# Kernel optimization log

Hardware: AMD Instinct MI355X
Metric: run time of the kernel (lower is better)

## Reference

```python
import jax, jax.numpy as jnp
import numpy as np

N = 8192
IN_DIM = 256
OUT_DIM = 256
NEG_INF = -9e15


def setup_inputs() -> dict:
    key = jax.random.key(0)
    k1, k2, k3, k4, k5 = jax.random.split(key, 5)
    worker_x = jax.random.normal(k1, (N, IN_DIM), dtype=jnp.float32)
    ww_adj = jax.random.randint(k2, (N, N), 0, 2, dtype=jnp.int32)
    # learned params (xavier-ish scales)
    W = jax.random.normal(k3, (IN_DIM, OUT_DIM), dtype=jnp.float32) * (1.0 / np.sqrt(IN_DIM))
    a_src = jax.random.normal(k4, (OUT_DIM, 1), dtype=jnp.float32) * (1.414 / np.sqrt(OUT_DIM))
    a_dst = jax.random.normal(k5, (OUT_DIM, 1), dtype=jnp.float32) * (1.414 / np.sqrt(OUT_DIM))
    return {"worker_x": worker_x, "ww_adj": ww_adj, "W": W, "a_src": a_src, "a_dst": a_dst}


def reference(worker_x, ww_adj, W, a_src, a_dst):
    Wh = worker_x @ W                       # [N, out_dim]
    f_src = Wh @ a_src                      # [N, 1]
    f_dst = Wh @ a_dst                      # [N, 1]
    e = jax.nn.leaky_relu(f_src + f_dst.T, negative_slope=0.2)  # [N, N]
    attention = jnp.where(ww_adj > 0, e, NEG_INF)
    attention = jax.nn.softmax(attention, axis=-1)
    h_prime = attention @ Wh                # [N, out_dim]
    return jax.nn.elu(h_prime)
```

## Files before the change

kernel.cpp:

```cpp
#include <hip/hip_runtime.h>
#include <stdint.h>

typedef __attribute__((ext_vector_type(8))) short short8;
typedef __attribute__((ext_vector_type(4))) float f32x4;
typedef __attribute__((ext_vector_type(4))) _Float16 h16x4;

#define LOG2E 1.4426950408889634f

#define OFF_WTT   0u
#define OFF_WHTB  131072u
#define OFF_BITS  4325376u
#define OFF_FSRC  12713984u
#define OFF_FDST  12746752u
#define OFF_MKEY  12779520u
#define OFF_LP    12779584u
#define OFF_ACCH  12910656u

__device__ __forceinline__ unsigned short f2bf(float f) {
    union { float f; unsigned int i; } v; v.f = f;
    unsigned int u = v.i;
    return (unsigned short)((u + 0x7FFFu + ((u >> 16) & 1u)) >> 16);
}


__global__ void k0_init(const float* __restrict__ W,
                        unsigned short* __restrict__ WTt,
                        unsigned int* __restrict__ Mkey) {
    int idx = blockIdx.x * 256 + threadIdx.x;
    int i = idx >> 8, o = idx & 255;
    WTt[(i >> 5) * 8192 + ((i >> 3) & 3) * 2048 + o * 8 + (i & 7)] = f2bf(W[idx]);
    if (idx == 0) *Mkey = 0u;
}

__global__ __launch_bounds__(256, 4)
void k_pack(const int* __restrict__ adj, unsigned int* __restrict__ bits) {
    int wave_id = (blockIdx.x * 256 + threadIdx.x) >> 6;
    int lane = threadIdx.x & 63;
#pragma unroll 2
    for (int it = 0; it < 64; ++it) {
        size_t win = (size_t)wave_id * 64 + it;
        int4 v = *(const int4*)(adj + win * 256 + lane * 4);
        unsigned int nib = (v.x > 0 ? 1u : 0u) | (v.y > 0 ? 2u : 0u) |
                           (v.z > 0 ? 4u : 0u) | (v.w > 0 ? 8u : 0u);
        unsigned int s;
        s = __shfl_xor(nib, 1, 64);  nib = (lane & 1) ? (s | (nib << 4))  : (nib | (s << 4));
        s = __shfl_xor(nib, 2, 64);  nib = (lane & 2) ? (s | (nib << 8))  : (nib | (s << 8));
        s = __shfl_xor(nib, 4, 64);  nib = (lane & 4) ? (s | (nib << 16)) : (nib | (s << 16));
        if ((lane & 7) == 0) bits[win * 8 + (lane >> 3)] = nib;
    }
}

__global__ __launch_bounds__(256, 2)
void k1_stage1(const float* __restrict__ X,
               const unsigned short* __restrict__ WTt,
               const float* __restrict__ a_src,
               const float* __restrict__ a_dst,
               unsigned short* __restrict__ WhTb,
               float* __restrict__ f_src,
               float* __restrict__ f_dst,
               unsigned int* __restrict__ Mkey) {
    __shared__ __align__(16) unsigned short Bt[8192];
    __shared__ float fsum[64];
    const int t = threadIdx.x, w = t >> 6, lane = t & 63, l15 = lane & 15, q = lane >> 4;
    const int rg = w & 1, cg = w >> 1;
    const int i0 = blockIdx.x * 32;
    const int arow = i0 + rg * 16 + l15;

    if (t < 64) fsum[t] = 0.f;

    float as[8], ad[8];
#pragma unroll
    for (int ci = 0; ci < 8; ++ci) {
        int col = cg * 128 + ci * 16 + l15;
        as[ci] = a_src[col]; ad[ci] = a_dst[col];
    }

    f32x4 acc[8];
#pragma unroll
    for (int ci = 0; ci < 8; ++ci) acc[ci] = (f32x4)0.f;

    for (int ks = 0; ks < 8; ++ks) {
        __syncthreads();
        {
            const uint4* src = (const uint4*)(WTt + ks * 8192);
            uint4* dst = (uint4*)Bt;
            dst[t] = src[t]; dst[256 + t] = src[256 + t];
            dst[512 + t] = src[512 + t]; dst[768 + t] = src[768 + t];
        }
        __syncthreads();
        const float* xp = X + (size_t)arow * 256 + ks * 32 + q * 8;
        float4 xa = *(const float4*)xp;
        float4 xb = *(const float4*)(xp + 4);
        short8 a;
        a[0] = (short)f2bf(xa.x); a[1] = (short)f2bf(xa.y);
        a[2] = (short)f2bf(xa.z); a[3] = (short)f2bf(xa.w);
        a[4] = (short)f2bf(xb.x); a[5] = (short)f2bf(xb.y);
        a[6] = (short)f2bf(xb.z); a[7] = (short)f2bf(xb.w);
#pragma unroll
        for (int ci = 0; ci < 8; ++ci) {
            short8 b = *(const short8*)((const char*)Bt + q * 4096 + (cg * 128 + ci * 16 + l15) * 16);
            acc[ci] = __builtin_amdgcn_mfma_f32_16x16x32_bf16(a, b, acc[ci], 0, 0, 0);
        }
    }

#pragma unroll
    for (int ci = 0; ci < 8; ++ci) {
        int col = cg * 128 + ci * 16 + l15;
        ushort4 v;
        v.x = f2bf(acc[ci][0]); v.y = f2bf(acc[ci][1]);
        v.z = f2bf(acc[ci][2]); v.w = f2bf(acc[ci][3]);
        size_t flat = (size_t)(i0 >> 5) * 8192 + (size_t)(rg * 2 + (q >> 1)) * 2048
                      + (size_t)col * 8 + (q & 1) * 4;
        *(ushort4*)(WhTb + flat) = v;
    }

#pragma unroll
    for (int reg = 0; reg < 4; ++reg) {
        float ps = 0.f, pd = 0.f;
#pragma unroll
        for (int ci = 0; ci < 8; ++ci) {
            ps += acc[ci][reg] * as[ci];
            pd += acc[ci][reg] * ad[ci];
        }
#pragma unroll
        for (int m = 1; m < 16; m <<= 1) {
            ps += __shfl_xor(ps, m, 64);
            pd += __shfl_xor(pd, m, 64);
        }
        if (l15 == 0) {
            atomicAdd(&fsum[rg * 16 + q * 4 + reg], ps);
            atomicAdd(&fsum[32 + rg * 16 + q * 4 + reg], pd);
        }
    }
    __syncthreads();
    if (t < 32) {
        int row = i0 + t;
        float ps = fsum[t], pd = fsum[32 + t];
        f_src[row] = ps;
        f_dst[row] = pd;
        union { float f; unsigned int u; } cv; cv.f = pd;
        unsigned int key = (cv.u & 0x80000000u) ? ~cv.u : (cv.u | 0x80000000u);
        atomicMax(Mkey, key);
    }
}

__global__ __launch_bounds__(512, 2)
void k2_flash(const unsigned int* __restrict__ BITS,
              const unsigned short* __restrict__ WhTb,
              const float* __restrict__ f_src,
              const float* __restrict__ f_dst,
              const unsigned int* __restrict__ Mkey,
              float* __restrict__ Lp,
              _Float16* __restrict__ ACCh) {
    __shared__ __align__(16) unsigned short Bt[2][8192];
    __shared__ float fd_s[2048];
    const int t = threadIdx.x, w = t >> 6, lane = t & 63, l15 = lane & 15, q = lane >> 4;
    const int rg = w >> 1, cg = w & 1;
    const int i0 = blockIdx.x * 128;
    const int jc = blockIdx.y;
    const int jb0 = jc * 2048, jw0 = jc * 64;
    const int rA = i0 + rg * 32 + l15, rB = rA + 16;

    unsigned int key = *Mkey;
    union { unsigned int u; float f; } mv;
    mv.u = (key & 0x80000000u) ? (key & 0x7FFFFFFFu) : ~key;
    const float Mf = mv.f;
    const float fsA = f_src[rA], fsB = f_src[rB];
    float vA = fsA + Mf; const float mcA = fmaxf(vA, 0.2f * vA) * LOG2E;
    float vB = fsB + Mf; const float mcB = fmaxf(vB, 0.2f * vB) * LOG2E;

    { float4* d = (float4*)fd_s; d[t] = *(const float4*)(f_dst + jb0 + t * 4); }
    {
        const uint4* src = (const uint4*)(WhTb + (size_t)jw0 * 8192);
        uint4* dst = (uint4*)&Bt[0][0];
        dst[t] = src[t]; dst[512 + t] = src[512 + t];
    }
    const unsigned int* bpA = BITS + (size_t)rA * 256 + jw0;
    const unsigned int* bpB = BITS + (size_t)rB * 256 + jw0;
    unsigned int pwA = bpA[0], pwB = bpB[0];

    f32x4 accA[8], accB[8];
#pragma unroll
    for (int ci = 0; ci < 8; ++ci) { accA[ci] = (f32x4)0.f; accB[ci] = (f32x4)0.f; }
    float lsA = 0.f, lsB = 0.f;
    __syncthreads();

    for (int js = 0; js < 64; ++js) {
        const int buf = js & 1;
        const int jn = (js + 1) & 63;
        const uint4* nsrc = (const uint4*)(WhTb + (size_t)(jw0 + jn) * 8192);
        uint4 g0 = nsrc[t];
        uint4 g1 = nsrc[512 + t];
        unsigned int nwA = bpA[jn], nwB = bpB[jn];

        const float* fdp = fd_s + js * 32 + q * 8;
        float4 f0 = *(const float4*)fdp, f1 = *(const float4*)(fdp + 4);
        float fdv[8] = { f0.x, f0.y, f0.z, f0.w, f1.x, f1.y, f1.z, f1.w };

        unsigned int bA = pwA >> (q * 8), bB = pwB >> (q * 8);
        short8 fragA, fragB;
#pragma unroll
        for (int k = 0; k < 8; ++k) {
            float tA = fsA + fdv[k];
            float eA = fmaxf(tA, 0.2f * tA);
            float pA = __builtin_amdgcn_exp2f(__builtin_fmaf(eA, LOG2E, -mcA));
            pA = ((bA >> k) & 1u) ? pA : 0.f;
            lsA += pA; fragA[k] = (short)f2bf(pA);
            float tB = fsB + fdv[k];
            float eB = fmaxf(tB, 0.2f * tB);
            float pB = __builtin_amdgcn_exp2f(__builtin_fmaf(eB, LOG2E, -mcB));
            pB = ((bB >> k) & 1u) ? pB : 0.f;
            lsB += pB; fragB[k] = (short)f2bf(pB);
        }

        const char* base = (const char*)&Bt[buf][0] + q * 4096 + (cg * 128 + l15) * 16;
#pragma unroll
        for (int ci = 0; ci < 8; ++ci) {
            short8 bf = *(const short8*)(base + ci * 256);
            accA[ci] = __builtin_amdgcn_mfma_f32_16x16x32_bf16(fragA, bf, accA[ci], 0, 0, 0);
            accB[ci] = __builtin_amdgcn_mfma_f32_16x16x32_bf16(fragB, bf, accB[ci], 0, 0, 0);
        }

        { uint4* dst = (uint4*)&Bt[buf ^ 1][0]; dst[t] = g0; dst[512 + t] = g1; }
        pwA = nwA; pwB = nwB;
        __syncthreads();
    }

    lsA += __shfl_xor(lsA, 16, 64); lsA += __shfl_xor(lsA, 32, 64);
    lsB += __shfl_xor(lsB, 16, 64); lsB += __shfl_xor(lsB, 32, 64);
    if (cg == 0 && q == 0) {
        Lp[(size_t)jc * 8192 + i0 + rg * 32 + l15] = lsA;
        Lp[(size_t)jc * 8192 + i0 + rg * 32 + 16 + l15] = lsB;
    }

    _Float16* ap = ACCh + (size_t)jc * 2097152;
#pragma unroll
    for (int ci = 0; ci < 8; ++ci) {
        int col = cg * 128 + ci * 16 + l15;
#pragma unroll
        for (int reg = 0; reg < 4; ++reg) {
            int rowA = i0 + rg * 32 + q * 4 + reg;
            ap[(size_t)rowA * 256 + col] = (_Float16)accA[ci][reg];
            ap[(size_t)(rowA + 16) * 256 + col] = (_Float16)accB[ci][reg];
        }
    }
}

__global__ void k4_final(const _Float16* __restrict__ ACCh,
                         const float* __restrict__ Lp,
                         float* __restrict__ out) {
    int gid = blockIdx.x * 256 + threadIdx.x;
    int i = gid >> 6;
    float s0 = 0.f, s1 = 0.f, s2 = 0.f, s3 = 0.f;
#pragma unroll
    for (int jc = 0; jc < 4; ++jc) {
        h16x4 v = *(const h16x4*)(ACCh + (size_t)jc * 2097152 + (size_t)gid * 4);
        s0 += (float)v[0]; s1 += (float)v[1]; s2 += (float)v[2]; s3 += (float)v[3];
    }
    float L = 0.f;
#pragma unroll
    for (int jc = 0; jc < 4; ++jc) L += Lp[jc * 8192 + i];
    float inv = (L > 0.f) ? (1.0f / L) : 0.f;
    float h0 = s0 * inv, h1 = s1 * inv, h2 = s2 * inv, h3 = s3 * inv;
    float4 o;
    o.x = (h0 > 0.f) ? h0 : expm1f(h0);
    o.y = (h1 > 0.f) ? h1 : expm1f(h1);
    o.z = (h2 > 0.f) ? h2 : expm1f(h2);
    o.w = (h3 > 0.f) ? h3 : expm1f(h3);
    *(float4*)(out + (size_t)gid * 4) = o;
}

extern "C" void kernel_launch(void* const* d_in, const int* in_sizes, int n_in,
                              void* d_out, int out_size, void* d_ws, size_t ws_size,
                              hipStream_t stream) {
    (void)in_sizes; (void)n_in; (void)out_size; (void)ws_size;
    const float* X   = (const float*)d_in[0];
    const int*   adj = (const int*)d_in[1];
    const float* W   = (const float*)d_in[2];
    const float* a_s = (const float*)d_in[3];
    const float* a_d = (const float*)d_in[4];

    char* ws = (char*)d_ws;
    unsigned short* WTt  = (unsigned short*)(ws + OFF_WTT);
    unsigned short* WhTb = (unsigned short*)(ws + OFF_WHTB);
    unsigned int*   BITS = (unsigned int*)(ws + OFF_BITS);
    float*          fsrc = (float*)(ws + OFF_FSRC);
    float*          fdst = (float*)(ws + OFF_FDST);
    unsigned int*   Mkey = (unsigned int*)(ws + OFF_MKEY);
    float*          Lp   = (float*)(ws + OFF_LP);
    _Float16*       ACCh = (_Float16*)(ws + OFF_ACCH);
    float*          out  = (float*)d_out;

    k0_init<<<dim3(256), dim3(256), 0, stream>>>(W, WTt, Mkey);
    k_pack<<<dim3(1024), dim3(256), 0, stream>>>(adj, BITS);
    k1_stage1<<<dim3(256), dim3(256), 0, stream>>>(X, WTt, a_s, a_d, WhTb, fsrc, fdst, Mkey);
    k2_flash<<<dim3(64, 4), dim3(512), 0, stream>>>(BITS, WhTb, fsrc, fdst, Mkey, Lp, ACCh);
    k4_final<<<dim3(2048), dim3(256), 0, stream>>>(ACCh, Lp, out);
}
```

Baseline: 487.2 us.

## Pack adjacency bits with wave ballots and retile flash kernel per-wave rows

The adjacency packing kernel now builds each 64-bit mask with a single wave ballot over scalar loads, replacing the nibble shuffle-reduction. The flash attention kernel shrinks to 256 threads and 64 rows per block, with each wave computing 16 rows across all 256 output columns, and the grid doubles. This removes the second row set per wave and the column split between waves. In exchange, each block reloads the value tiles for fewer rows, and LDS reads per MFMA increase.

Result: faster. 459.4 us (-5.7%).

```diff
diff --git a/kernel.cpp b/kernel.cpp
--- a/kernel.cpp
+++ b/kernel.cpp
@@ -22,7 +22,6 @@
     return (unsigned short)((u + 0x7FFFu + ((u >> 16) & 1u)) >> 16);
 }
 
-
 __global__ void k0_init(const float* __restrict__ W,
                         unsigned short* __restrict__ WTt,
                         unsigned int* __restrict__ Mkey) {
@@ -32,21 +31,21 @@
     if (idx == 0) *Mkey = 0u;
 }
 
-__global__ __launch_bounds__(256, 4)
-void k_pack(const int* __restrict__ adj, unsigned int* __restrict__ bits) {
+__global__ __launch_bounds__(256, 8)
+void k_pack(const int* __restrict__ adj, unsigned long long* __restrict__ bits64) {
     int wave_id = (blockIdx.x * 256 + threadIdx.x) >> 6;
     int lane = threadIdx.x & 63;
-#pragma unroll 2
-    for (int it = 0; it < 64; ++it) {
-        size_t win = (size_t)wave_id * 64 + it;
-        int4 v = *(const int4*)(adj + win * 256 + lane * 4);
-        unsigned int nib = (v.x > 0 ? 1u : 0u) | (v.y > 0 ? 2u : 0u) |
-                           (v.z > 0 ? 4u : 0u) | (v.w > 0 ? 8u : 0u);
-        unsigned int s;
-        s = __shfl_xor(nib, 1, 64);  nib = (lane & 1) ? (s | (nib << 4))  : (nib | (s << 4));
-        s = __shfl_xor(nib, 2, 64);  nib = (lane & 2) ? (s | (nib << 8))  : (nib | (s << 8));
-        s = __shfl_xor(nib, 4, 64);  nib = (lane & 4) ? (s | (nib << 16)) : (nib | (s << 16));
-        if ((lane & 7) == 0) bits[win * 8 + (lane >> 3)] = nib;
+    const int* p = adj + (size_t)wave_id * 16384 + lane;
+    unsigned long long* bp = bits64 + (size_t)wave_id * 256;
+    for (int it = 0; it < 256; it += 8) {
+        int v[8];
+#pragma unroll
+        for (int u = 0; u < 8; ++u) v[u] = p[(size_t)(it + u) * 64];
+#pragma unroll
+        for (int u = 0; u < 8; ++u) {
+            unsigned long long m = __ballot(v[u] > 0);
+            if (lane == 0) bp[it + u] = m;
+        }
     }
 }
 
@@ -144,7 +143,7 @@
     }
 }
 
-__global__ __launch_bounds__(512, 2)
+__global__ __launch_bounds__(256, 4)
 void k2_flash(const unsigned int* __restrict__ BITS,
               const unsigned short* __restrict__ WhTb,
               const float* __restrict__ f_src,
@@ -155,50 +154,51 @@
     __shared__ __align__(16) unsigned short Bt[2][8192];
     __shared__ float fd_s[2048];
     const int t = threadIdx.x, w = t >> 6, lane = t & 63, l15 = lane & 15, q = lane >> 4;
-    const int rg = w >> 1, cg = w & 1;
-    const int i0 = blockIdx.x * 128;
+    const int i0 = blockIdx.x * 64;
     const int jc = blockIdx.y;
     const int jb0 = jc * 2048, jw0 = jc * 64;
-    const int rA = i0 + rg * 32 + l15, rB = rA + 16;
+    const int rA = i0 + w * 16 + l15;
 
     unsigned int key = *Mkey;
     union { unsigned int u; float f; } mv;
     mv.u = (key & 0x80000000u) ? (key & 0x7FFFFFFFu) : ~key;
     const float Mf = mv.f;
-    const float fsA = f_src[rA], fsB = f_src[rB];
+    const float fsA = f_src[rA];
     float vA = fsA + Mf; const float mcA = fmaxf(vA, 0.2f * vA) * LOG2E;
-    float vB = fsB + Mf; const float mcB = fmaxf(vB, 0.2f * vB) * LOG2E;
-
-    { float4* d = (float4*)fd_s; d[t] = *(const float4*)(f_dst + jb0 + t * 4); }
+
+    {
+        float4* d = (float4*)fd_s;
+        const float4* src = (const float4*)(f_dst + jb0);
+        d[t] = src[t]; d[256 + t] = src[256 + t];
+    }
     {
         const uint4* src = (const uint4*)(WhTb + (size_t)jw0 * 8192);
         uint4* dst = (uint4*)&Bt[0][0];
-        dst[t] = src[t]; dst[512 + t] = src[512 + t];
+        dst[t] = src[t]; dst[256 + t] = src[256 + t];
+        dst[512 + t] = src[512 + t]; dst[768 + t] = src[768 + t];
     }
     const unsigned int* bpA = BITS + (size_t)rA * 256 + jw0;
-    const unsigned int* bpB = BITS + (size_t)rB * 256 + jw0;
-    unsigned int pwA = bpA[0], pwB = bpB[0];
-
-    f32x4 accA[8], accB[8];
-#pragma unroll
-    for (int ci = 0; ci < 8; ++ci) { accA[ci] = (f32x4)0.f; accB[ci] = (f32x4)0.f; }
-    float lsA = 0.f, lsB = 0.f;
+    unsigned int pwA = bpA[0];
+
+    f32x4 acc[16];
+#pragma unroll
+    for (int ci = 0; ci < 16; ++ci) acc[ci] = (f32x4)0.f;
+    float lsA = 0.f;
     __syncthreads();
 
     for (int js = 0; js < 64; ++js) {
         const int buf = js & 1;
         const int jn = (js + 1) & 63;
         const uint4* nsrc = (const uint4*)(WhTb + (size_t)(jw0 + jn) * 8192);
-        uint4 g0 = nsrc[t];
-        uint4 g1 = nsrc[512 + t];
-        unsigned int nwA = bpA[jn], nwB = bpB[jn];
+        uint4 g0 = nsrc[t], g1 = nsrc[256 + t], g2 = nsrc[512 + t], g3 = nsrc[768 + t];
+        unsigned int nwA = bpA[jn];
 
         const float* fdp = fd_s + js * 32 + q * 8;
         float4 f0 = *(const float4*)fdp, f1 = *(const float4*)(fdp + 4);
         float fdv[8] = { f0.x, f0.y, f0.z, f0.w, f1.x, f1.y, f1.z, f1.w };
 
-        unsigned int bA = pwA >> (q * 8), bB = pwB >> (q * 8);
-        short8 fragA, fragB;
+        unsigned int bA = pwA >> (q * 8);
+        short8 fragA;
 #pragma unroll
         for (int k = 0; k < 8; ++k) {
             float tA = fsA + fdv[k];
@@ -206,42 +206,31 @@
             float pA = __builtin_amdgcn_exp2f(__builtin_fmaf(eA, LOG2E, -mcA));
             pA = ((bA >> k) & 1u) ? pA : 0.f;
             lsA += pA; fragA[k] = (short)f2bf(pA);
-            float tB = fsB + fdv[k];
-            float eB = fmaxf(tB, 0.2f * tB);
-            float pB = __builtin_amdgcn_exp2f(__builtin_fmaf(eB, LOG2E, -mcB));
-            pB = ((bB >> k) & 1u) ? pB : 0.f;
-            lsB += pB; fragB[k] = (short)f2bf(pB);
-        }
-
-        const char* base = (const char*)&Bt[buf][0] + q * 4096 + (cg * 128 + l15) * 16;
-#pragma unroll
-        for (int ci = 0; ci < 8; ++ci) {
+        }
+
+        const char* base = (const char*)&Bt[buf][0] + q * 4096 + l15 * 16;
+#pragma unroll
+        for (int ci = 0; ci < 16; ++ci) {
             short8 bf = *(const short8*)(base + ci * 256);
-            accA[ci] = __builtin_amdgcn_mfma_f32_16x16x32_bf16(fragA, bf, accA[ci], 0, 0, 0);
-            accB[ci] = __builtin_amdgcn_mfma_f32_16x16x32_bf16(fragB, bf, accB[ci], 0, 0, 0);
-        }
-
-        { uint4* dst = (uint4*)&Bt[buf ^ 1][0]; dst[t] = g0; dst[512 + t] = g1; }
-        pwA = nwA; pwB = nwB;
+            acc[ci] = __builtin_amdgcn_mfma_f32_16x16x32_bf16(fragA, bf, acc[ci], 0, 0, 0);
+        }
+
+        { uint4* dst = (uint4*)&Bt[buf ^ 1][0];
+          dst[t] = g0; dst[256 + t] = g1; dst[512 + t] = g2; dst[768 + t] = g3; }
+        pwA = nwA;
         __syncthreads();
     }
 
     lsA += __shfl_xor(lsA, 16, 64); lsA += __shfl_xor(lsA, 32, 64);
-    lsB += __shfl_xor(lsB, 16, 64); lsB += __shfl_xor(lsB, 32, 64);
-    if (cg == 0 && q == 0) {
-        Lp[(size_t)jc * 8192 + i0 + rg * 32 + l15] = lsA;
-        Lp[(size_t)jc * 8192 + i0 + rg * 32 + 16 + l15] = lsB;
-    }
+    if (lane < 16) Lp[(size_t)jc * 8192 + i0 + w * 16 + lane] = lsA;
 
     _Float16* ap = ACCh + (size_t)jc * 2097152;
 #pragma unroll
-    for (int ci = 0; ci < 8; ++ci) {
-        int col = cg * 128 + ci * 16 + l15;
+    for (int ci = 0; ci < 16; ++ci) {
 #pragma unroll
         for (int reg = 0; reg < 4; ++reg) {
-            int rowA = i0 + rg * 32 + q * 4 + reg;
-            ap[(size_t)rowA * 256 + col] = (_Float16)accA[ci][reg];
-            ap[(size_t)(rowA + 16) * 256 + col] = (_Float16)accB[ci][reg];
+            int row = i0 + w * 16 + q * 4 + reg;
+            ap[(size_t)row * 256 + ci * 16 + l15] = (_Float16)acc[ci][reg];
         }
     }
 }
@@ -283,6 +272,7 @@
     char* ws = (char*)d_ws;
     unsigned short* WTt  = (unsigned short*)(ws + OFF_WTT);
     unsigned short* WhTb = (unsigned short*)(ws + OFF_WHTB);
+    unsigned long long* B64 = (unsigned long long*)(ws + OFF_BITS);
     unsigned int*   BITS = (unsigned int*)(ws + OFF_BITS);
     float*          fsrc = (float*)(ws + OFF_FSRC);
     float*          fdst = (float*)(ws + OFF_FDST);
@@ -292,8 +282,8 @@
     float*          out  = (float*)d_out;
 
     k0_init<<<dim3(256), dim3(256), 0, stream>>>(W, WTt, Mkey);
-    k_pack<<<dim3(1024), dim3(256), 0, stream>>>(adj, BITS);
+    k_pack<<<dim3(1024), dim3(256), 0, stream>>>(adj, B64);
     k1_stage1<<<dim3(256), dim3(256), 0, stream>>>(X, WTt, a_s, a_d, WhTb, fsrc, fdst, Mkey);
-    k2_flash<<<dim3(64, 4), dim3(512), 0, stream>>>(BITS, WhTb, fsrc, fdst, Mkey, Lp, ACCh);
+    k2_flash<<<dim3(128, 4), dim3(256), 0, stream>>>(BITS, WhTb, fsrc, fdst, Mkey, Lp, ACCh);
     k4_final<<<dim3(2048), dim3(256), 0, stream>>>(ACCh, Lp, out);
 }
```
